# Kernel optimization log

Hardware: AMD Instinct MI355X
Metric: run time of the kernel (lower is better)

The kernel has to match this reference:

```python
import jax, jax.numpy as jnp
import numpy as np

B, K = 4096, 64
D_MODEL, D_DYN, D_STAT = 256, 512, 64
H = 4
DH = D_MODEL // H
SCALE = DH ** -0.5
LN_EPS = 1e-5


def _ln(x, g, b):
    m = x.mean(-1, keepdims=True)
    v = ((x - m) ** 2).mean(-1, keepdims=True)
    return (x - m) * jax.lax.rsqrt(v + LN_EPS) * g + b


def setup_inputs() -> dict:
    key = jax.random.key(0)
    ks = jax.random.split(key, 16)
    w = lambda k, s: jax.random.normal(k, s, jnp.float32) * 0.02
    return {
        "h_dyn": jax.random.normal(ks[0], (B, D_DYN), jnp.float32),
        "x_stat": jax.random.normal(ks[1], (B, K, D_STAT), jnp.float32),
        "W_dyn": w(ks[2], (D_DYN, D_MODEL)), "b_dyn": jnp.zeros((D_MODEL,)),
        "W_stat": w(ks[3], (D_STAT, D_MODEL)), "b_stat": jnp.zeros((D_MODEL,)),
        "g_ndyn": jnp.ones((D_MODEL,)), "b_ndyn": jnp.zeros((D_MODEL,)),
        "g_nstat": jnp.ones((D_MODEL,)), "b_nstat": jnp.zeros((D_MODEL,)),
        "Wq": w(ks[4], (D_MODEL, D_MODEL)), "bq": jnp.zeros((D_MODEL,)),
        "Wk": w(ks[5], (D_MODEL, D_MODEL)), "bk": jnp.zeros((D_MODEL,)),
        "Wv": w(ks[6], (D_MODEL, D_MODEL)), "bv": jnp.zeros((D_MODEL,)),
        "g_mlp": jnp.ones((D_MODEL,)), "b_mlp": jnpp if False else jnp.zeros((D_MODEL,)),
        "W1": w(ks[7], (D_MODEL, D_MODEL)), "b1": jnp.zeros((D_MODEL,)),
        "W2": w(ks[8], (D_MODEL, D_MODEL)), "b2": jnp.zeros((D_MODEL,)),
        "Wo": w(ks[9], (D_MODEL, D_MODEL)), "bo": jnp.zeros((D_MODEL,)),
        "res_scale": jnp.float32(0.1),
    }


def reference(h_dyn, x_stat, W_dyn, b_dyn, W_stat, b_stat, g_ndyn, b_ndyn,
              g_nstat, b_nstat, Wq, bq, Wk, bk, Wv, bv, g_mlp, b_mlp,
              W1, b1, W2, b2, Wo, bo, res_scale):
    h0 = h_dyn @ W_dyn + b_dyn                  # [B, d_model]
    s = x_stat @ W_stat + b_stat                # [B, K, d_model]
    h = _ln(h0, g_ndyn, b_ndyn)
    s = _ln(s, g_nstat, b_nstat)

    q = (h @ Wq + bq).reshape(B, H, DH)         # [B, H, dh]
    k = (s @ Wk + bk).reshape(B, K, H, DH)      # [B, K, H, dh]
    v_flat = s @ Wv + bv                        # [B, K, d_model]

    # per-variable MLP (DeepSets style): LN -> Linear -> GELU(exact) -> Linear
    t = _ln(v_flat, g_mlp, b_mlp)
    t = jax.nn.gelu(t @ W1 + b1, approximate=False)
    v_tokens = t @ W2 + b2                      # [B, K, d_model]

    logits = jnp.einsum('bhd,bkhd->bhk', q, k) * SCALE   # [B, H, K]
    w = jax.nn.sigmoid(logits)
    w = w / (w.sum(-1, keepdims=True) + 1e-6)

    vh = v_tokens.reshape(B, K, H, DH)
    z = jnp.einsum('bhk,bkhd->bhd', w, vh).reshape(B, D_MODEL)
    c = z @ Wo + bo
    c = h0 + res_scale * c
    w_mean = w.mean(axis=1)                     # [B, K]
    return c, w_mean
```

## Files before the change

kernel.cpp:

```cpp
#include <hip/hip_runtime.h>
#include <cmath>


typedef __bf16 bf16;
typedef bf16 bf16x4 __attribute__((ext_vector_type(4)));
typedef bf16 bf16x8 __attribute__((ext_vector_type(8)));
typedef float f32x4 __attribute__((ext_vector_type(4)));

#define MFMA_B16(a, b, c) __builtin_amdgcn_mfma_f32_16x16x32_bf16((a), (b), (c), 0, 0, 0)

constexpr int SROW = 264;

constexpr size_t WSTAT_P = 0;
constexpr size_t WV_P    = 16384;
constexpr size_t W1_P    = 81920;
constexpr size_t W2O_P   = 147456;
constexpr size_t WDYN_P  = 212992;
constexpr size_t WQ_P    = 344064;
constexpr size_t WK_P    = 409600;
constexpr size_t KQ_BF   = 475136;
constexpr size_t XP_BF   = 4669440;
constexpr size_t H0_F   = 10723328;
constexpr size_t BKQ_F  = 11771904;
constexpr size_t B2O_F  = 11788288;
constexpr size_t W2OS_F = 11788544;

__device__ __forceinline__ bf16x8 zero8() {
  bf16x8 z;
#pragma unroll
  for (int j = 0; j < 8; ++j) z[j] = (bf16)0.0f;
  return z;
}

__device__ __forceinline__ float wave_sum(float v) {
#pragma unroll
  for (int m = 1; m < 64; m <<= 1) v += __shfl_xor(v, m, 64);
  return v;
}

__device__ __forceinline__ void zero_acc(f32x4 (&acc)[4][4]) {
#pragma unroll
  for (int mt = 0; mt < 4; ++mt)
#pragma unroll
    for (int nt = 0; nt < 4; ++nt) { f32x4 z = {0.f, 0.f, 0.f, 0.f}; acc[mt][nt] = z; }
}

__device__ __forceinline__ void gemm_swapped_p(const bf16* buf, const bf16* __restrict__ Wp,
                                               int w, int lane, int l16, int koff,
                                               f32x4 (&acc)[4][4]) {
  const bf16* base = Wp + (size_t)w * 8 * 2048 + lane * 8;
  bf16x8 aw[2][4];
#pragma unroll
  for (int dt = 0; dt < 4; ++dt) aw[0][dt] = *(const bf16x8*)(base + dt * 512);
#pragma unroll
  for (int ks = 0; ks < 8; ++ks) {
    const int cur = ks & 1;
    if (ks < 7) {
#pragma unroll
      for (int dt = 0; dt < 4; ++dt)
        aw[cur ^ 1][dt] = *(const bf16x8*)(base + (ks + 1) * 2048 + dt * 512);
    }
#pragma unroll
    for (int tt = 0; tt < 4; ++tt) {
      bf16x8 bfrag = *(const bf16x8*)(buf + (tt * 16 + l16) * SROW + ks * 32 + koff);
#pragma unroll
      for (int dt = 0; dt < 4; ++dt) acc[dt][tt] = MFMA_B16(aw[cur][dt], bfrag, acc[dt][tt]);
    }
  }
}

__device__ __forceinline__ void gemm_orig_p(const bf16* buf, const bf16* __restrict__ Wp,
                                            int w, int lane, int l16, int koff,
                                            f32x4 (&acc)[4][4]) {
  const bf16* base = Wp + (size_t)w * 8 * 2048 + lane * 8;
  bf16x8 bw[2][4];
#pragma unroll
  for (int nt = 0; nt < 4; ++nt) bw[0][nt] = *(const bf16x8*)(base + nt * 512);
#pragma unroll
  for (int ks = 0; ks < 8; ++ks) {
    const int cur = ks & 1;
    if (ks < 7) {
#pragma unroll
      for (int nt = 0; nt < 4; ++nt)
        bw[cur ^ 1][nt] = *(const bf16x8*)(base + (ks + 1) * 2048 + nt * 512);
    }
#pragma unroll
    for (int mt = 0; mt < 4; ++mt) {
      bf16x8 a = *(const bf16x8*)(buf + (mt * 16 + l16) * SROW + ks * 32 + koff);
#pragma unroll
      for (int nt = 0; nt < 4; ++nt) acc[mt][nt] = MFMA_B16(a, bw[cur][nt], acc[mt][nt]);
    }
  }
}

__device__ __forceinline__ void store_swapped_stats(bf16* buf, const float* __restrict__ bsrc,
                                                    f32x4 (&acc)[4][4], int w, int quad, int l16,
                                                    float (*part_s)[64], float (*part_ss)[64]) {
  float ps[4] = {0.f, 0.f, 0.f, 0.f}, pq[4] = {0.f, 0.f, 0.f, 0.f};
#pragma unroll
  for (int dt = 0; dt < 4; ++dt) {
    const float4 bb = *(const float4*)(bsrc + w * 64 + dt * 16 + quad * 4);
#pragma unroll
    for (int tt = 0; tt < 4; ++tt) {
      float v0 = acc[dt][tt][0] + bb.x;
      float v1 = acc[dt][tt][1] + bb.y;
      float v2 = acc[dt][tt][2] + bb.z;
      float v3 = acc[dt][tt][3] + bb.w;
      ps[tt] += (v0 + v1) + (v2 + v3);
      pq[tt] += v0 * v0 + v1 * v1 + v2 * v2 + v3 * v3;
      bf16x4 o;
      o[0] = (bf16)v0; o[1] = (bf16)v1; o[2] = (bf16)v2; o[3] = (bf16)v3;
      *(bf16x4*)(buf + (tt * 16 + l16) * SROW + w * 64 + dt * 16 + quad * 4) = o;
    }
  }
#pragma unroll
  for (int tt = 0; tt < 4; ++tt) {
    ps[tt] += __shfl_xor(ps[tt], 16, 64); ps[tt] += __shfl_xor(ps[tt], 32, 64);
    pq[tt] += __shfl_xor(pq[tt], 16, 64); pq[tt] += __shfl_xor(pq[tt], 32, 64);
  }
  if (quad == 0) {
#pragma unroll
    for (int tt = 0; tt < 4; ++tt) {
      part_s[w][tt * 16 + l16] = ps[tt];
      part_ss[w][tt * 16 + l16] = pq[tt];
    }
  }
}

__device__ __forceinline__ void ln_finalize_apply(bf16* buf, const float* __restrict__ g,
                                                  const float* __restrict__ bsh,
                                                  const float (*part_s)[64],
                                                  const float (*part_ss)[64], int w, int lane) {
  float psum = (part_s[0][lane] + part_s[1][lane]) + (part_s[2][lane] + part_s[3][lane]);
  float pqq  = (part_ss[0][lane] + part_ss[1][lane]) + (part_ss[2][lane] + part_ss[3][lane]);
  float mean = psum * (1.f / 256.f);
  float var  = pqq * (1.f / 256.f) - mean * mean;
  float rstd = 1.f / sqrtf(var + 1e-5f);
  const float4 gv = *(const float4*)(g + lane * 4);
  const float4 bv4 = *(const float4*)(bsh + lane * 4);
#pragma unroll
  for (int i = 0; i < 16; ++i) {
    const int row = 4 * i + w;
    const float mb = __shfl(mean, row, 64);
    const float rb = __shfl(rstd, row, 64);
    bf16* rp = buf + row * SROW + lane * 4;
    bf16x4 xv = *(const bf16x4*)rp;
    bf16x4 o;
    o[0] = (bf16)(((float)xv[0] - mb) * rb * gv.x + bv4.x);
    o[1] = (bf16)(((float)xv[1] - mb) * rb * gv.y + bv4.y);
    o[2] = (bf16)(((float)xv[2] - mb) * rb * gv.z + bv4.z);
    o[3] = (bf16)(((float)xv[3] - mb) * rb * gv.w + bv4.w);
    *(bf16x4*)rp = o;
  }
}

template <typename SrcT>
__device__ __forceinline__ void pack_slice(const SrcT* __restrict__ src, bf16* __restrict__ dstb,
                                           int w, int ks, bool trans, float* sh, int tid) {
  if (!trans) {
#pragma unroll
    for (int i = 0; i < 8; ++i) {
      int r = i * 4 + (tid >> 6), c = tid & 63;
      sh[r * 65 + c] = (float)src[(size_t)(ks * 32 + r) * 256 + w * 64 + c];
    }
  } else {
    int c = tid >> 2, j8 = tid & 3;
#pragma unroll
    for (int jj = 0; jj < 8; ++jj) {
      int r = j8 * 8 + jj;
      sh[r * 65 + c] = (float)src[(size_t)(w * 64 + c) * 256 + ks * 32 + r];
    }
  }
  __syncthreads();
  const int x = tid >> 6, quad = (tid >> 4) & 3, l16 = tid & 15;
  bf16x8 o;
#pragma unroll
  for (int j = 0; j < 8; ++j) o[j] = (bf16)sh[(quad * 8 + j) * 65 + x * 16 + l16];
  *(bf16x8*)(dstb + tid * 8) = o;
}

__global__ void prep1_kernel(const float* __restrict__ x_stat,
                             const float* __restrict__ Wdyn, const float* __restrict__ Wstat,
                             const float* __restrict__ Wq, const float* __restrict__ Wk,
                             const float* __restrict__ Wv, const float* __restrict__ W1,
                             const float* __restrict__ W2, const float* __restrict__ Wo,
                             const float* __restrict__ b2,
                             bf16* __restrict__ ws, float* __restrict__ wsf) {
  __shared__ float sh[64 * 65];
  __shared__ float part[4][8];
  const int idx = blockIdx.x;
  const int tid = threadIdx.x;

  if (idx < 4096) {
    const float* xb = x_stat + (size_t)idx * 4096;
#pragma unroll
    for (int j = 0; j < 4; ++j) {
      int lin = j * 1024 + tid * 4;
      float4 v = *(const float4*)(xb + lin);
      int r = lin >> 6, c = lin & 63;
      sh[r * 65 + c] = v.x; sh[r * 65 + c + 1] = v.y;
      sh[r * 65 + c + 2] = v.z; sh[r * 65 + c + 3] = v.w;
    }
    __syncthreads();
    bf16* xp = ws + XP_BF + (size_t)idx * 4096;
#pragma unroll
    for (int half = 0; half < 2; ++half) {
      int s = half * 256 + tid;
      int ksq = s >> 6, lane = s & 63;
      int token = (ksq & 3) * 16 + (lane & 15);
      int f0 = (ksq >> 2) * 32 + (lane >> 4) * 8;
      bf16x8 o;
#pragma unroll
      for (int j = 0; j < 8; ++j) o[j] = (bf16)sh[token * 65 + f0 + j];
      *(bf16x8*)(xp + s * 8) = o;
    }
    return;
  }

  if (idx < 4128) {
    const int n0 = (idx - 4096) * 8;
    float4 a0 = *(const float4*)(Wo + (size_t)tid * 256 + n0);
    float4 a1 = *(const float4*)(Wo + (size_t)tid * 256 + n0 + 4);
    sh[tid * 8 + 0] = a0.x; sh[tid * 8 + 1] = a0.y; sh[tid * 8 + 2] = a0.z; sh[tid * 8 + 3] = a0.w;
    sh[tid * 8 + 4] = a1.x; sh[tid * 8 + 5] = a1.y; sh[tid * 8 + 6] = a1.z; sh[tid * 8 + 7] = a1.w;
    __syncthreads();
    float acc[8] = {0.f, 0.f, 0.f, 0.f, 0.f, 0.f, 0.f, 0.f};
    const float* row = W2 + (size_t)tid * 256;
    for (int d0 = 0; d0 < 256; d0 += 4) {
      float4 wv = *(const float4*)(row + d0);
#pragma unroll
      for (int dd = 0; dd < 4; ++dd) {
        float r = (dd == 0) ? wv.x : (dd == 1) ? wv.y : (dd == 2) ? wv.z : wv.w;
        const float* cc = &sh[(d0 + dd) * 8];
#pragma unroll
        for (int j = 0; j < 8; ++j) acc[j] += r * cc[j];
      }
    }
    float* dst = wsf + W2OS_F;
#pragma unroll
    for (int j = 0; j < 8; ++j) dst[(size_t)tid * 256 + n0 + j] = acc[j];
    const int w = tid >> 6, lane = tid & 63;
    float bval = b2[tid];
#pragma unroll
    for (int j = 0; j < 8; ++j) {
      float p = wave_sum(bval * sh[tid * 8 + j]);
      if (lane == 0) part[w][j] = p;
    }
    __syncthreads();
    if (tid < 8)
      wsf[B2O_F + n0 + tid] = part[0][tid] + part[1][tid] + part[2][tid] + part[3][tid];
    return;
  }

  int t = idx - 4128;
  const float* src; bf16* dst; int KS; bool trans = false;
  if (t < 64)       { src = Wdyn;  dst = ws + WDYN_P;  KS = 16; }
  else if (t < 72)  { src = Wstat; dst = ws + WSTAT_P; KS = 2;  t -= 64; }
  else if (t < 104) { src = Wq;    dst = ws + WQ_P;    KS = 8;  t -= 72; }
  else if (t < 136) { src = Wv;    dst = ws + WV_P;    KS = 8;  t -= 104; }
  else if (t < 168) { src = W1;    dst = ws + W1_P;    KS = 8;  t -= 136; }
  else              { src = Wk;    dst = ws + WK_P;    KS = 8;  t -= 168; trans = true; }
  const int w = t / KS, ks = t % KS;
  pack_slice<float>(src, dst + (size_t)(w * KS + ks) * 2048, w, ks, trans, sh, tid);
}

__global__ void prep2_kernel(const float* __restrict__ wsf_scr, bf16* __restrict__ ws) {
  __shared__ float sh[64 * 65];
  const int t = blockIdx.x;
  const int w = t >> 3, ks = t & 7;
  pack_slice<float>(wsf_scr, ws + W2O_P + (size_t)(w * 8 + ks) * 2048, w, ks, false, sh,
                    threadIdx.x);
}

__launch_bounds__(256, 2)
__global__ void pre_kernel(const float* __restrict__ h_dyn, const float* __restrict__ b_dyn,
                           const float* __restrict__ g_ndyn, const float* __restrict__ b_ndyn,
                           const float* __restrict__ bq, const float* __restrict__ bk,
                           const bf16* __restrict__ Wdyn_p, const bf16* __restrict__ Wq_p,
                           const bf16* __restrict__ Wk_p,
                           float* __restrict__ h0_out, bf16* __restrict__ kq_out,
                           float* __restrict__ bkq_out) {
  __shared__ float h0t[8][264];
  __shared__ bf16 hlnt[8][264];
  __shared__ bf16 qt[8][264];
  const int tid = threadIdx.x;
  const int w = tid >> 6, lane = tid & 63, quad = lane >> 4, l16 = lane & 15;
  const int koff = quad * 8;
  const int b0 = blockIdx.x * 8;
  const int mrow = l16 & 7;

  {
    f32x4 acc[4];
#pragma unroll
    for (int nt = 0; nt < 4; ++nt) { f32x4 z = {0.f, 0.f, 0.f, 0.f}; acc[nt] = z; }
    const float* arow = h_dyn + (size_t)(b0 + mrow) * 512;
    const bf16* base = Wdyn_p + (size_t)w * 16 * 2048 + lane * 8;
    for (int ks = 0; ks < 16; ++ks) {
      float4 x0 = *(const float4*)(arow + ks * 32 + koff);
      float4 x1 = *(const float4*)(arow + ks * 32 + koff + 4);
      bf16x8 a;
      a[0] = (bf16)x0.x; a[1] = (bf16)x0.y; a[2] = (bf16)x0.z; a[3] = (bf16)x0.w;
      a[4] = (bf16)x1.x; a[5] = (bf16)x1.y; a[6] = (bf16)x1.z; a[7] = (bf16)x1.w;
#pragma unroll
      for (int nt = 0; nt < 4; ++nt) {
        bf16x8 bw = *(const bf16x8*)(base + ks * 2048 + nt * 512);
        acc[nt] = MFMA_B16(a, bw, acc[nt]);
      }
    }
    if (quad < 2) {
#pragma unroll
      for (int nt = 0; nt < 4; ++nt) {
        int col = w * 64 + nt * 16 + l16;
        float bb = b_dyn[col];
#pragma unroll
        for (int r = 0; r < 4; ++r) {
          int row = quad * 4 + r;
          float v = acc[nt][r] + bb;
          h0t[row][col] = v;
          h0_out[(size_t)(b0 + row) * 256 + col] = v;
        }
      }
    }
  }
  __syncthreads();

  {
    float gn[4], bn[4];
#pragma unroll
    for (int j = 0; j < 4; ++j) { gn[j] = g_ndyn[lane + 64 * j]; bn[j] = b_ndyn[lane + 64 * j]; }
#pragma unroll
    for (int i = 0; i < 2; ++i) {
      int row = 4 * i + w;
      float x[4]; float s = 0.f, ss = 0.f;
#pragma unroll
      for (int j = 0; j < 4; ++j) { x[j] = h0t[row][lane + 64 * j]; s += x[j]; ss += x[j] * x[j]; }
      s = wave_sum(s); ss = wave_sum(ss);
      float mean = s * (1.f / 256.f);
      float var = ss * (1.f / 256.f) - mean * mean;
      float rstd = 1.f / sqrtf(var + 1e-5f);
#pragma unroll
      for (int j = 0; j < 4; ++j)
        hlnt[row][lane + 64 * j] = (bf16)((x[j] - mean) * rstd * gn[j] + bn[j]);
    }
  }
  __syncthreads();

  {
    f32x4 acc[4];
#pragma unroll
    for (int nt = 0; nt < 4; ++nt) { f32x4 z = {0.f, 0.f, 0.f, 0.f}; acc[nt] = z; }
    const bf16* base = Wq_p + (size_t)w * 8 * 2048 + lane * 8;
    for (int ks = 0; ks < 8; ++ks) {
      bf16x8 a = *(const bf16x8*)(&hlnt[mrow][ks * 32 + koff]);
#pragma unroll
      for (int nt = 0; nt < 4; ++nt) {
        bf16x8 bw = *(const bf16x8*)(base + ks * 2048 + nt * 512);
        acc[nt] = MFMA_B16(a, bw, acc[nt]);
      }
    }
    if (quad < 2) {
#pragma unroll
      for (int nt = 0; nt < 4; ++nt) {
        int col = w * 64 + nt * 16 + l16;
        float bb = bq[col];
#pragma unroll
        for (int r = 0; r < 4; ++r)
          qt[quad * 4 + r][col] = (bf16)(acc[nt][r] + bb);
      }
    }
  }
  __syncthreads();

  {
    const int pair = tid >> 2;
    const int row = pair >> 2, h = pair & 3, sub = tid & 3;
    if (row < 8) {
      float p = 0.f;
#pragma unroll
      for (int j = 0; j < 16; ++j) {
        int e = sub * 16 + j;
        p += (float)qt[row][h * 64 + e] * bk[h * 64 + e];
      }
      p += __shfl_xor(p, 1, 64);
      p += __shfl_xor(p, 2, 64);
      if (sub == 0) bkq_out[(size_t)(b0 + row) * 4 + h] = p;
    }
  }

  for (int h = 0; h < 4; ++h) {
    f32x4 acc[4];
#pragma unroll
    for (int nt = 0; nt < 4; ++nt) { f32x4 z = {0.f, 0.f, 0.f, 0.f}; acc[nt] = z; }
    const bf16* base = Wk_p + (size_t)w * 8 * 2048 + lane * 8;
#pragma unroll
    for (int ks = 0; ks < 2; ++ks) {
      bf16x8 a = *(const bf16x8*)(&qt[mrow][h * 64 + ks * 32 + koff]);
#pragma unroll
      for (int nt = 0; nt < 4; ++nt) {
        bf16x8 bw = *(const bf16x8*)(base + (h * 2 + ks) * 2048 + nt * 512);
        acc[nt] = MFMA_B16(a, bw, acc[nt]);
      }
    }
    if (quad < 2) {
#pragma unroll
      for (int nt = 0; nt < 4; ++nt)
#pragma unroll
        for (int r = 0; r < 4; ++r)
          kq_out[(size_t)(b0 + quad * 4 + r) * 1024 + h * 256 + w * 64 + nt * 16 + l16] =
              (bf16)acc[nt][r];
    }
  }
}

__launch_bounds__(256, 4)
__global__ void fused_kernel(
    const float* __restrict__ b_stat,
    const float* __restrict__ g_nstat, const float* __restrict__ b_nstat,
    const float* __restrict__ bv, const float* __restrict__ g_mlp,
    const float* __restrict__ b_mlp, const float* __restrict__ b1,
    const float* __restrict__ bo, const float* __restrict__ res_scale_p,
    const float* __restrict__ h0g, const float* __restrict__ bkq_g,
    const float* __restrict__ b2o_g,
    const bf16* __restrict__ Wstat_p, const bf16* __restrict__ Wv_p,
    const bf16* __restrict__ W1_p, const bf16* __restrict__ W2o_p,
    const bf16* __restrict__ kq_g, const bf16* __restrict__ xp_g,
    float* __restrict__ out_c, float* __restrict__ out_wm) {

  __shared__ bf16 buf[64 * SROW];
  __shared__ float part_s[4][64];
  __shared__ float part_ss[4][64];
  __shared__ float watt[4][64];
  __shared__ float swh[4];

  const int b = blockIdx.x;
  const int tid = threadIdx.x;
  const int w = tid >> 6, lane = tid & 63, quad = lane >> 4, l16 = lane & 15;
  const int koff = quad * 8;

  {
    f32x4 acc[4][4];
    zero_acc(acc);
    const bf16* xp_b = xp_g + (size_t)b * 4096 + lane * 8;
    const bf16* wsb = Wstat_p + (size_t)w * 2 * 2048 + lane * 8;
#pragma unroll
    for (int ks = 0; ks < 2; ++ks) {
      bf16x8 aw[4];
#pragma unroll
      for (int dt = 0; dt < 4; ++dt)
        aw[dt] = *(const bf16x8*)(wsb + ks * 2048 + dt * 512);
#pragma unroll
      for (int tt = 0; tt < 4; ++tt) {
        bf16x8 bfrag = *(const bf16x8*)(xp_b + (ks * 4 + tt) * 512);
#pragma unroll
        for (int dt = 0; dt < 4; ++dt) acc[dt][tt] = MFMA_B16(aw[dt], bfrag, acc[dt][tt]);
      }
    }
    store_swapped_stats(buf, b_stat, acc, w, quad, l16, part_s, part_ss);
  }
  __syncthreads();

  ln_finalize_apply(buf, g_nstat, b_nstat, part_s, part_ss, w, lane);
  __syncthreads();

  {
    const bf16* kq_b = kq_g + (size_t)b * 1024;
    f32x4 accL = {0.f, 0.f, 0.f, 0.f};
#pragma unroll
    for (int ks = 0; ks < 8; ++ks) {
      bf16x8 a = *(const bf16x8*)(buf + (w * 16 + l16) * SROW + ks * 32 + koff);
      bf16x8 kf = zero8();
      if (l16 < 4) kf = *(const bf16x8*)(kq_b + l16 * 256 + ks * 32 + koff);
      accL = MFMA_B16(a, kf, accL);
    }
    float bkqv = (l16 < 4) ? bkq_g[(size_t)b * 4 + l16] : 0.f;
#pragma unroll
    for (int r = 0; r < 4; ++r) {
      float lg = (accL[r] + bkqv) * 0.125f;
      float sig = 1.f / (1.f + __expf(-lg));
      if (l16 < 4) watt[l16][w * 16 + quad * 4 + r] = sig;
    }
  }

  {
    f32x4 acc[4][4];
    zero_acc(acc);
    gemm_swapped_p(buf, Wv_p, w, lane, l16, koff, acc);
    __syncthreads();
    {
      float v = watt[w][lane];
      float den = wave_sum(v);
      float dinv = 1.f / (den + 1e-6f);
      watt[w][lane] = v * dinv;
      if (lane == 0) swh[w] = den * dinv;
    }
    store_swapped_stats(buf, bv, acc, w, quad, l16, part_s, part_ss);
  }
  __syncthreads();

  if (tid < 64)
    out_wm[(size_t)b * 64 + tid] =
        0.25f * (watt[0][tid] + watt[1][tid] + watt[2][tid] + watt[3][tid]);
  ln_finalize_apply(buf, g_mlp, b_mlp, part_s, part_ss, w, lane);
  __syncthreads();

  {
    f32x4 acc[4][4];
    zero_acc(acc);
    gemm_swapped_p(buf, W1_p, w, lane, l16, koff, acc);
    __syncthreads();
#pragma unroll
    for (int dt = 0; dt < 4; ++dt) {
      const float4 bb = *(const float4*)(b1 + w * 64 + dt * 16 + quad * 4);
#pragma unroll
      for (int tt = 0; tt < 4; ++tt) {
        float v0 = acc[dt][tt][0] + bb.x;
        float v1 = acc[dt][tt][1] + bb.y;
        float v2 = acc[dt][tt][2] + bb.z;
        float v3 = acc[dt][tt][3] + bb.w;
        bf16x4 o;
        o[0] = (bf16)(v0 / (1.f + __expf(-1.702f * v0)));
        o[1] = (bf16)(v1 / (1.f + __expf(-1.702f * v1)));
        o[2] = (bf16)(v2 / (1.f + __expf(-1.702f * v2)));
        o[3] = (bf16)(v3 / (1.f + __expf(-1.702f * v3)));
        *(bf16x4*)(buf + (tt * 16 + l16) * SROW + w * 64 + dt * 16 + quad * 4) = o;
      }
    }
  }
  __syncthreads();

  {
    f32x4 acc[4][4];
    zero_acc(acc);
    gemm_orig_p(buf, W2o_p, w, lane, l16, koff, acc);
    float zacc[4] = {0.f, 0.f, 0.f, 0.f};
#pragma unroll
    for (int mt = 0; mt < 4; ++mt)
#pragma unroll
      for (int r = 0; r < 4; ++r) {
        float wt = watt[w][mt * 16 + quad * 4 + r];
#pragma unroll
        for (int nt = 0; nt < 4; ++nt) zacc[nt] += wt * acc[mt][nt][r];
      }
#pragma unroll
    for (int nt = 0; nt < 4; ++nt) {
      zacc[nt] += __shfl_xor(zacc[nt], 16, 64);
      zacc[nt] += __shfl_xor(zacc[nt], 32, 64);
    }
    if (quad == 0) {
      float rs = *res_scale_p;
#pragma unroll
      for (int nt = 0; nt < 4; ++nt) {
        int col = w * 64 + nt * 16 + l16;
        float res = zacc[nt] + swh[w] * b2o_g[col] + bo[col];
        out_c[(size_t)b * 256 + col] = h0g[(size_t)b * 256 + col] + rs * res;
      }
    }
  }
}

extern "C" void kernel_launch(void* const* d_in, const int* in_sizes, int n_in,
                              void* d_out, int out_size, void* d_ws, size_t ws_size,
                              hipStream_t stream) {
  const float* h_dyn   = (const float*)d_in[0];
  const float* x_stat  = (const float*)d_in[1];
  const float* W_dyn   = (const float*)d_in[2];
  const float* b_dyn   = (const float*)d_in[3];
  const float* W_stat  = (const float*)d_in[4];
  const float* b_stat  = (const float*)d_in[5];
  const float* g_ndyn  = (const float*)d_in[6];
  const float* b_ndyn  = (const float*)d_in[7];
  const float* g_nstat = (const float*)d_in[8];
  const float* b_nstat = (const float*)d_in[9];
  const float* Wq = (const float*)d_in[10];
  const float* bq = (const float*)d_in[11];
  const float* Wk = (const float*)d_in[12];
  const float* bk = (const float*)d_in[13];
  const float* Wv = (const float*)d_in[14];
  const float* bv = (const float*)d_in[15];
  const float* g_mlp = (const float*)d_in[16];
  const float* b_mlp = (const float*)d_in[17];
  const float* W1 = (const float*)d_in[18];
  const float* b1 = (const float*)d_in[19];
  const float* W2 = (const float*)d_in[20];
  const float* b2 = (const float*)d_in[21];
  const float* Wo = (const float*)d_in[22];
  const float* bo = (const float*)d_in[23];
  const float* rs = (const float*)d_in[24];

  bf16* ws = (bf16*)d_ws;
  float* wsf = (float*)d_ws;

  prep1_kernel<<<4328, 256, 0, stream>>>(x_stat, W_dyn, W_stat, Wq, Wk, Wv, W1, W2, Wo, b2,
                                         ws, wsf);
  prep2_kernel<<<32, 256, 0, stream>>>(wsf + W2OS_F, ws);

  pre_kernel<<<512, 256, 0, stream>>>(h_dyn, b_dyn, g_ndyn, b_ndyn, bq, bk,
                                      ws + WDYN_P, ws + WQ_P, ws + WK_P,
                                      wsf + H0_F, ws + KQ_BF, wsf + BKQ_F);

  float* out_c = (float*)d_out;
  float* out_wm = out_c + (size_t)4096 * 256;
  fused_kernel<<<4096, 256, 0, stream>>>(
      b_stat, g_nstat, b_nstat, bv, g_mlp, b_mlp, b1, bo, rs,
      wsf + H0_F, wsf + BKQ_F, wsf + B2O_F,
      ws + WSTAT_P, ws + WV_P, ws + W1_P, ws + W2O_P,
      ws + KQ_BF, ws + XP_BF,
      out_c, out_wm);
}
```

Baseline: 340.0 us.

## Process two batches per block, load x_stat directly, drop prepacked x buffer

The fused kernel now handles two batch items per block (128 token rows), so each weight fragment loaded from global memory is reused across twice as many MFMA tiles. The separate prep pass that converted x_stat to packed bf16 in the workspace is removed. x_stat is instead read as fp32 and converted into LDS inside the fused kernel, which saves a full write and reread of that tensor. The pre_kernel GEMMs also get double-buffered weight loads. In exchange, LDS roughly doubles, the accumulator arrays grow to 32 tiles, and occupancy drops to 2 blocks per CU with a risk of register pressure.

Measured after the change: 328.3 us. 3.5% less time.

```diff
diff --git a/kernel.cpp b/kernel.cpp
--- a/kernel.cpp
+++ b/kernel.cpp
@@ -10,6 +10,7 @@
 #define MFMA_B16(a, b, c) __builtin_amdgcn_mfma_f32_16x16x32_bf16((a), (b), (c), 0, 0, 0)
 
 constexpr int SROW = 264;
+constexpr int XROW = 72;
 
 constexpr size_t WSTAT_P = 0;
 constexpr size_t WV_P    = 16384;
@@ -19,11 +20,10 @@
 constexpr size_t WQ_P    = 344064;
 constexpr size_t WK_P    = 409600;
 constexpr size_t KQ_BF   = 475136;
-constexpr size_t XP_BF   = 4669440;
-constexpr size_t H0_F   = 10723328;
-constexpr size_t BKQ_F  = 11771904;
-constexpr size_t B2O_F  = 11788288;
-constexpr size_t W2OS_F = 11788544;
+constexpr size_t H0_F   = 2334720;
+constexpr size_t BKQ_F  = 3383296;
+constexpr size_t B2O_F  = 3399680;
+constexpr size_t W2OS_F = 3399936;
 
 __device__ __forceinline__ bf16x8 zero8() {
   bf16x8 z;
@@ -38,16 +38,9 @@
   return v;
 }
 
-__device__ __forceinline__ void zero_acc(f32x4 (&acc)[4][4]) {
-#pragma unroll
-  for (int mt = 0; mt < 4; ++mt)
-#pragma unroll
-    for (int nt = 0; nt < 4; ++nt) { f32x4 z = {0.f, 0.f, 0.f, 0.f}; acc[mt][nt] = z; }
-}
-
-__device__ __forceinline__ void gemm_swapped_p(const bf16* buf, const bf16* __restrict__ Wp,
-                                               int w, int lane, int l16, int koff,
-                                               f32x4 (&acc)[4][4]) {
+__device__ __forceinline__ void gemm_swapped8(const bf16* buf, const bf16* __restrict__ Wp,
+                                              int w, int lane, int l16, int koff,
+                                              f32x4 (&acc)[4][8]) {
   const bf16* base = Wp + (size_t)w * 8 * 2048 + lane * 8;
   bf16x8 aw[2][4];
 #pragma unroll
@@ -61,7 +54,7 @@
         aw[cur ^ 1][dt] = *(const bf16x8*)(base + (ks + 1) * 2048 + dt * 512);
     }
 #pragma unroll
-    for (int tt = 0; tt < 4; ++tt) {
+    for (int tt = 0; tt < 8; ++tt) {
       bf16x8 bfrag = *(const bf16x8*)(buf + (tt * 16 + l16) * SROW + ks * 32 + koff);
 #pragma unroll
       for (int dt = 0; dt < 4; ++dt) acc[dt][tt] = MFMA_B16(aw[cur][dt], bfrag, acc[dt][tt]);
@@ -69,9 +62,9 @@
   }
 }
 
-__device__ __forceinline__ void gemm_orig_p(const bf16* buf, const bf16* __restrict__ Wp,
-                                            int w, int lane, int l16, int koff,
-                                            f32x4 (&acc)[4][4]) {
+__device__ __forceinline__ void gemm_orig8(const bf16* buf, const bf16* __restrict__ Wp,
+                                           int w, int lane, int l16, int koff,
+                                           f32x4 (&acc)[8][4]) {
   const bf16* base = Wp + (size_t)w * 8 * 2048 + lane * 8;
   bf16x8 bw[2][4];
 #pragma unroll
@@ -85,7 +78,7 @@
         bw[cur ^ 1][nt] = *(const bf16x8*)(base + (ks + 1) * 2048 + nt * 512);
     }
 #pragma unroll
-    for (int mt = 0; mt < 4; ++mt) {
+    for (int mt = 0; mt < 8; ++mt) {
       bf16x8 a = *(const bf16x8*)(buf + (mt * 16 + l16) * SROW + ks * 32 + koff);
 #pragma unroll
       for (int nt = 0; nt < 4; ++nt) acc[mt][nt] = MFMA_B16(a, bw[cur][nt], acc[mt][nt]);
@@ -93,15 +86,17 @@
   }
 }
 
-__device__ __forceinline__ void store_swapped_stats(bf16* buf, const float* __restrict__ bsrc,
-                                                    f32x4 (&acc)[4][4], int w, int quad, int l16,
-                                                    float (*part_s)[64], float (*part_ss)[64]) {
-  float ps[4] = {0.f, 0.f, 0.f, 0.f}, pq[4] = {0.f, 0.f, 0.f, 0.f};
+__device__ __forceinline__ void store_stats8(bf16* buf, const float* __restrict__ bsrc,
+                                             f32x4 (&acc)[4][8], int w, int quad, int l16,
+                                             float (*part_s)[4][64], float (*part_ss)[4][64]) {
+  float ps[8], pq[8];
+#pragma unroll
+  for (int tt = 0; tt < 8; ++tt) { ps[tt] = 0.f; pq[tt] = 0.f; }
 #pragma unroll
   for (int dt = 0; dt < 4; ++dt) {
     const float4 bb = *(const float4*)(bsrc + w * 64 + dt * 16 + quad * 4);
 #pragma unroll
-    for (int tt = 0; tt < 4; ++tt) {
+    for (int tt = 0; tt < 8; ++tt) {
       float v0 = acc[dt][tt][0] + bb.x;
       float v1 = acc[dt][tt][1] + bb.y;
       float v2 = acc[dt][tt][2] + bb.z;
@@ -114,61 +109,67 @@
     }
   }
 #pragma unroll
-  for (int tt = 0; tt < 4; ++tt) {
+  for (int tt = 0; tt < 8; ++tt) {
     ps[tt] += __shfl_xor(ps[tt], 16, 64); ps[tt] += __shfl_xor(ps[tt], 32, 64);
     pq[tt] += __shfl_xor(pq[tt], 16, 64); pq[tt] += __shfl_xor(pq[tt], 32, 64);
   }
   if (quad == 0) {
 #pragma unroll
-    for (int tt = 0; tt < 4; ++tt) {
-      part_s[w][tt * 16 + l16] = ps[tt];
-      part_ss[w][tt * 16 + l16] = pq[tt];
-    }
-  }
-}
-
-__device__ __forceinline__ void ln_finalize_apply(bf16* buf, const float* __restrict__ g,
-                                                  const float* __restrict__ bsh,
-                                                  const float (*part_s)[64],
-                                                  const float (*part_ss)[64], int w, int lane) {
-  float psum = (part_s[0][lane] + part_s[1][lane]) + (part_s[2][lane] + part_s[3][lane]);
-  float pqq  = (part_ss[0][lane] + part_ss[1][lane]) + (part_ss[2][lane] + part_ss[3][lane]);
-  float mean = psum * (1.f / 256.f);
-  float var  = pqq * (1.f / 256.f) - mean * mean;
-  float rstd = 1.f / sqrtf(var + 1e-5f);
+    for (int tt = 0; tt < 8; ++tt) {
+      part_s[tt >> 2][w][(tt & 3) * 16 + l16] = ps[tt];
+      part_ss[tt >> 2][w][(tt & 3) * 16 + l16] = pq[tt];
+    }
+  }
+}
+
+__device__ __forceinline__ void ln_apply2(bf16* buf, const float* __restrict__ g,
+                                          const float* __restrict__ bsh,
+                                          const float (*ps)[4][64], const float (*pss)[4][64],
+                                          int w, int lane) {
+  float mean[2], rstd[2];
+#pragma unroll
+  for (int bb = 0; bb < 2; ++bb) {
+    float s = (ps[bb][0][lane] + ps[bb][1][lane]) + (ps[bb][2][lane] + ps[bb][3][lane]);
+    float q = (pss[bb][0][lane] + pss[bb][1][lane]) + (pss[bb][2][lane] + pss[bb][3][lane]);
+    mean[bb] = s * (1.f / 256.f);
+    float var = q * (1.f / 256.f) - mean[bb] * mean[bb];
+    rstd[bb] = 1.f / sqrtf(var + 1e-5f);
+  }
   const float4 gv = *(const float4*)(g + lane * 4);
   const float4 bv4 = *(const float4*)(bsh + lane * 4);
 #pragma unroll
-  for (int i = 0; i < 16; ++i) {
-    const int row = 4 * i + w;
-    const float mb = __shfl(mean, row, 64);
-    const float rb = __shfl(rstd, row, 64);
-    bf16* rp = buf + row * SROW + lane * 4;
-    bf16x4 xv = *(const bf16x4*)rp;
-    bf16x4 o;
-    o[0] = (bf16)(((float)xv[0] - mb) * rb * gv.x + bv4.x);
-    o[1] = (bf16)(((float)xv[1] - mb) * rb * gv.y + bv4.y);
-    o[2] = (bf16)(((float)xv[2] - mb) * rb * gv.z + bv4.z);
-    o[3] = (bf16)(((float)xv[3] - mb) * rb * gv.w + bv4.w);
-    *(bf16x4*)rp = o;
-  }
-}
-
-template <typename SrcT>
-__device__ __forceinline__ void pack_slice(const SrcT* __restrict__ src, bf16* __restrict__ dstb,
+  for (int bb = 0; bb < 2; ++bb) {
+#pragma unroll
+    for (int i = 0; i < 16; ++i) {
+      const int r64 = 4 * i + w;
+      const float mb = __shfl(mean[bb], r64, 64);
+      const float rb = __shfl(rstd[bb], r64, 64);
+      bf16* rp = buf + (bb * 64 + r64) * SROW + lane * 4;
+      bf16x4 xv = *(const bf16x4*)rp;
+      bf16x4 o;
+      o[0] = (bf16)(((float)xv[0] - mb) * rb * gv.x + bv4.x);
+      o[1] = (bf16)(((float)xv[1] - mb) * rb * gv.y + bv4.y);
+      o[2] = (bf16)(((float)xv[2] - mb) * rb * gv.z + bv4.z);
+      o[3] = (bf16)(((float)xv[3] - mb) * rb * gv.w + bv4.w);
+      *(bf16x4*)rp = o;
+    }
+  }
+}
+
+__device__ __forceinline__ void pack_slice(const float* __restrict__ src, bf16* __restrict__ dstb,
                                            int w, int ks, bool trans, float* sh, int tid) {
   if (!trans) {
 #pragma unroll
     for (int i = 0; i < 8; ++i) {
       int r = i * 4 + (tid >> 6), c = tid & 63;
-      sh[r * 65 + c] = (float)src[(size_t)(ks * 32 + r) * 256 + w * 64 + c];
+      sh[r * 65 + c] = src[(size_t)(ks * 32 + r) * 256 + w * 64 + c];
     }
   } else {
     int c = tid >> 2, j8 = tid & 3;
 #pragma unroll
     for (int jj = 0; jj < 8; ++jj) {
       int r = j8 * 8 + jj;
-      sh[r * 65 + c] = (float)src[(size_t)(w * 64 + c) * 256 + ks * 32 + r];
+      sh[r * 65 + c] = src[(size_t)(w * 64 + c) * 256 + ks * 32 + r];
     }
   }
   __syncthreads();
@@ -179,8 +180,7 @@
   *(bf16x8*)(dstb + tid * 8) = o;
 }
 
-__global__ void prep1_kernel(const float* __restrict__ x_stat,
-                             const float* __restrict__ Wdyn, const float* __restrict__ Wstat,
+__global__ void prep1_kernel(const float* __restrict__ Wdyn, const float* __restrict__ Wstat,
                              const float* __restrict__ Wq, const float* __restrict__ Wk,
                              const float* __restrict__ Wv, const float* __restrict__ W1,
                              const float* __restrict__ W2, const float* __restrict__ Wo,
@@ -191,34 +191,8 @@
   const int idx = blockIdx.x;
   const int tid = threadIdx.x;
 
-  if (idx < 4096) {
-    const float* xb = x_stat + (size_t)idx * 4096;
-#pragma unroll
-    for (int j = 0; j < 4; ++j) {
-      int lin = j * 1024 + tid * 4;
-      float4 v = *(const float4*)(xb + lin);
-      int r = lin >> 6, c = lin & 63;
-      sh[r * 65 + c] = v.x; sh[r * 65 + c + 1] = v.y;
-      sh[r * 65 + c + 2] = v.z; sh[r * 65 + c + 3] = v.w;
-    }
-    __syncthreads();
-    bf16* xp = ws + XP_BF + (size_t)idx * 4096;
-#pragma unroll
-    for (int half = 0; half < 2; ++half) {
-      int s = half * 256 + tid;
-      int ksq = s >> 6, lane = s & 63;
-      int token = (ksq & 3) * 16 + (lane & 15);
-      int f0 = (ksq >> 2) * 32 + (lane >> 4) * 8;
-      bf16x8 o;
-#pragma unroll
-      for (int j = 0; j < 8; ++j) o[j] = (bf16)sh[token * 65 + f0 + j];
-      *(bf16x8*)(xp + s * 8) = o;
-    }
-    return;
-  }
-
-  if (idx < 4128) {
-    const int n0 = (idx - 4096) * 8;
+  if (idx < 32) {
+    const int n0 = idx * 8;
     float4 a0 = *(const float4*)(Wo + (size_t)tid * 256 + n0);
     float4 a1 = *(const float4*)(Wo + (size_t)tid * 256 + n0 + 4);
     sh[tid * 8 + 0] = a0.x; sh[tid * 8 + 1] = a0.y; sh[tid * 8 + 2] = a0.z; sh[tid * 8 + 3] = a0.w;
@@ -252,7 +226,7 @@
     return;
   }
 
-  int t = idx - 4128;
+  int t = idx - 32;
   const float* src; bf16* dst; int KS; bool trans = false;
   if (t < 64)       { src = Wdyn;  dst = ws + WDYN_P;  KS = 16; }
   else if (t < 72)  { src = Wstat; dst = ws + WSTAT_P; KS = 2;  t -= 64; }
@@ -261,15 +235,13 @@
   else if (t < 168) { src = W1;    dst = ws + W1_P;    KS = 8;  t -= 136; }
   else              { src = Wk;    dst = ws + WK_P;    KS = 8;  t -= 168; trans = true; }
   const int w = t / KS, ks = t % KS;
-  pack_slice<float>(src, dst + (size_t)(w * KS + ks) * 2048, w, ks, trans, sh, tid);
+  pack_slice(src, dst + (size_t)(w * KS + ks) * 2048, w, ks, trans, sh, tid);
 }
 
 __global__ void prep2_kernel(const float* __restrict__ wsf_scr, bf16* __restrict__ ws) {
   __shared__ float sh[64 * 65];
   const int t = blockIdx.x;
-  const int w = t >> 3, ks = t & 7;
-  pack_slice<float>(wsf_scr, ws + W2O_P + (size_t)(w * 8 + ks) * 2048, w, ks, false, sh,
-                    threadIdx.x);
+  pack_slice(wsf_scr, ws + W2O_P + (size_t)t * 2048, t >> 3, t & 7, false, sh, threadIdx.x);
 }
 
 __launch_bounds__(256, 2)
@@ -295,17 +267,23 @@
     for (int nt = 0; nt < 4; ++nt) { f32x4 z = {0.f, 0.f, 0.f, 0.f}; acc[nt] = z; }
     const float* arow = h_dyn + (size_t)(b0 + mrow) * 512;
     const bf16* base = Wdyn_p + (size_t)w * 16 * 2048 + lane * 8;
+    bf16x8 bw[2][4];
+#pragma unroll
+    for (int nt = 0; nt < 4; ++nt) bw[0][nt] = *(const bf16x8*)(base + nt * 512);
     for (int ks = 0; ks < 16; ++ks) {
+      const int cur = ks & 1;
+      if (ks < 15) {
+#pragma unroll
+        for (int nt = 0; nt < 4; ++nt)
+          bw[cur ^ 1][nt] = *(const bf16x8*)(base + (ks + 1) * 2048 + nt * 512);
+      }
       float4 x0 = *(const float4*)(arow + ks * 32 + koff);
       float4 x1 = *(const float4*)(arow + ks * 32 + koff + 4);
       bf16x8 a;
       a[0] = (bf16)x0.x; a[1] = (bf16)x0.y; a[2] = (bf16)x0.z; a[3] = (bf16)x0.w;
       a[4] = (bf16)x1.x; a[5] = (bf16)x1.y; a[6] = (bf16)x1.z; a[7] = (bf16)x1.w;
 #pragma unroll
-      for (int nt = 0; nt < 4; ++nt) {
-        bf16x8 bw = *(const bf16x8*)(base + ks * 2048 + nt * 512);
-        acc[nt] = MFMA_B16(a, bw, acc[nt]);
-      }
+      for (int nt = 0; nt < 4; ++nt) acc[nt] = MFMA_B16(a, bw[cur][nt], acc[nt]);
     }
     if (quad < 2) {
 #pragma unroll
@@ -350,13 +328,19 @@
 #pragma unroll
     for (int nt = 0; nt < 4; ++nt) { f32x4 z = {0.f, 0.f, 0.f, 0.f}; acc[nt] = z; }
     const bf16* base = Wq_p + (size_t)w * 8 * 2048 + lane * 8;
+    bf16x8 bw[2][4];
+#pragma unroll
+    for (int nt = 0; nt < 4; ++nt) bw[0][nt] = *(const bf16x8*)(base + nt * 512);
     for (int ks = 0; ks < 8; ++ks) {
+      const int cur = ks & 1;
+      if (ks < 7) {
+#pragma unroll
+        for (int nt = 0; nt < 4; ++nt)
+          bw[cur ^ 1][nt] = *(const bf16x8*)(base + (ks + 1) * 2048 + nt * 512);
+      }
       bf16x8 a = *(const bf16x8*)(&hlnt[mrow][ks * 32 + koff]);
 #pragma unroll
-      for (int nt = 0; nt < 4; ++nt) {
-        bf16x8 bw = *(const bf16x8*)(base + ks * 2048 + nt * 512);
-        acc[nt] = MFMA_B16(a, bw, acc[nt]);
-      }
+      for (int nt = 0; nt < 4; ++nt) acc[nt] = MFMA_B16(a, bw[cur][nt], acc[nt]);
     }
     if (quad < 2) {
 #pragma unroll
@@ -412,9 +396,9 @@
   }
 }
 
-__launch_bounds__(256, 4)
+__launch_bounds__(256, 2)
 __global__ void fused_kernel(
-    const float* __restrict__ b_stat,
+    const float* __restrict__ x_stat, const float* __restrict__ b_stat,
     const float* __restrict__ g_nstat, const float* __restrict__ b_nstat,
     const float* __restrict__ bv, const float* __restrict__ g_mlp,
     const float* __restrict__ b_mlp, const float* __restrict__ b1,
@@ -423,96 +407,124 @@
     const float* __restrict__ b2o_g,
     const bf16* __restrict__ Wstat_p, const bf16* __restrict__ Wv_p,
     const bf16* __restrict__ W1_p, const bf16* __restrict__ W2o_p,
-    const bf16* __restrict__ kq_g, const bf16* __restrict__ xp_g,
+    const bf16* __restrict__ kq_g,
     float* __restrict__ out_c, float* __restrict__ out_wm) {
 
-  __shared__ bf16 buf[64 * SROW];
-  __shared__ float part_s[4][64];
-  __shared__ float part_ss[4][64];
-  __shared__ float watt[4][64];
-  __shared__ float swh[4];
-
-  const int b = blockIdx.x;
+  __shared__ bf16 buf[128 * SROW];
+  __shared__ float part_s[2][4][64];
+  __shared__ float part_ss[2][4][64];
+  __shared__ float watt[2][4][64];
+  __shared__ float swh[2][4];
+
+  const int b0 = blockIdx.x * 2;
   const int tid = threadIdx.x;
   const int w = tid >> 6, lane = tid & 63, quad = lane >> 4, l16 = lane & 15;
   const int koff = quad * 8;
 
-  {
-    f32x4 acc[4][4];
-    zero_acc(acc);
-    const bf16* xp_b = xp_g + (size_t)b * 4096 + lane * 8;
+  bf16* xs = buf;
+  {
+    const float* xb = x_stat + (size_t)b0 * 4096;
+#pragma unroll
+    for (int j = 0; j < 8; ++j) {
+      int idx = j * 1024 + tid * 4;
+      float4 v = *(const float4*)(xb + idx);
+      bf16x4 o;
+      o[0] = (bf16)v.x; o[1] = (bf16)v.y; o[2] = (bf16)v.z; o[3] = (bf16)v.w;
+      *(bf16x4*)(xs + (idx >> 6) * XROW + (idx & 63)) = o;
+    }
+  }
+  __syncthreads();
+
+  {
+    f32x4 acc[4][8];
+#pragma unroll
+    for (int dt = 0; dt < 4; ++dt)
+#pragma unroll
+      for (int tt = 0; tt < 8; ++tt) { f32x4 z = {0.f, 0.f, 0.f, 0.f}; acc[dt][tt] = z; }
     const bf16* wsb = Wstat_p + (size_t)w * 2 * 2048 + lane * 8;
-#pragma unroll
-    for (int ks = 0; ks < 2; ++ks) {
-      bf16x8 aw[4];
+    bf16x8 aw[2][4];
+#pragma unroll
+    for (int ks = 0; ks < 2; ++ks)
 #pragma unroll
       for (int dt = 0; dt < 4; ++dt)
-        aw[dt] = *(const bf16x8*)(wsb + ks * 2048 + dt * 512);
-#pragma unroll
-      for (int tt = 0; tt < 4; ++tt) {
-        bf16x8 bfrag = *(const bf16x8*)(xp_b + (ks * 4 + tt) * 512);
-#pragma unroll
-        for (int dt = 0; dt < 4; ++dt) acc[dt][tt] = MFMA_B16(aw[dt], bfrag, acc[dt][tt]);
-      }
-    }
-    store_swapped_stats(buf, b_stat, acc, w, quad, l16, part_s, part_ss);
-  }
-  __syncthreads();
-
-  ln_finalize_apply(buf, g_nstat, b_nstat, part_s, part_ss, w, lane);
-  __syncthreads();
-
-  {
-    const bf16* kq_b = kq_g + (size_t)b * 1024;
+        aw[ks][dt] = *(const bf16x8*)(wsb + ks * 2048 + dt * 512);
+#pragma unroll
+    for (int ks = 0; ks < 2; ++ks)
+#pragma unroll
+      for (int tt = 0; tt < 8; ++tt) {
+        bf16x8 bfrag = *(const bf16x8*)(xs + (tt * 16 + l16) * XROW + ks * 32 + koff);
+#pragma unroll
+        for (int dt = 0; dt < 4; ++dt) acc[dt][tt] = MFMA_B16(aw[ks][dt], bfrag, acc[dt][tt]);
+      }
+    __syncthreads();
+    store_stats8(buf, b_stat, acc, w, quad, l16, part_s, part_ss);
+  }
+  __syncthreads();
+
+  ln_apply2(buf, g_nstat, b_nstat, part_s, part_ss, w, lane);
+  __syncthreads();
+
+#pragma unroll
+  for (int bb = 0; bb < 2; ++bb) {
+    const bf16* kq_b = kq_g + (size_t)(b0 + bb) * 1024;
     f32x4 accL = {0.f, 0.f, 0.f, 0.f};
 #pragma unroll
     for (int ks = 0; ks < 8; ++ks) {
-      bf16x8 a = *(const bf16x8*)(buf + (w * 16 + l16) * SROW + ks * 32 + koff);
+      bf16x8 a = *(const bf16x8*)(buf + (bb * 64 + w * 16 + l16) * SROW + ks * 32 + koff);
       bf16x8 kf = zero8();
       if (l16 < 4) kf = *(const bf16x8*)(kq_b + l16 * 256 + ks * 32 + koff);
       accL = MFMA_B16(a, kf, accL);
     }
-    float bkqv = (l16 < 4) ? bkq_g[(size_t)b * 4 + l16] : 0.f;
+    float bkqv = (l16 < 4) ? bkq_g[(size_t)(b0 + bb) * 4 + l16] : 0.f;
 #pragma unroll
     for (int r = 0; r < 4; ++r) {
       float lg = (accL[r] + bkqv) * 0.125f;
       float sig = 1.f / (1.f + __expf(-lg));
-      if (l16 < 4) watt[l16][w * 16 + quad * 4 + r] = sig;
-    }
-  }
-
-  {
-    f32x4 acc[4][4];
-    zero_acc(acc);
-    gemm_swapped_p(buf, Wv_p, w, lane, l16, koff, acc);
+      if (l16 < 4) watt[bb][l16][w * 16 + quad * 4 + r] = sig;
+    }
+  }
+
+  {
+    f32x4 acc[4][8];
+#pragma unroll
+    for (int dt = 0; dt < 4; ++dt)
+#pragma unroll
+      for (int tt = 0; tt < 8; ++tt) { f32x4 z = {0.f, 0.f, 0.f, 0.f}; acc[dt][tt] = z; }
+    gemm_swapped8(buf, Wv_p, w, lane, l16, koff, acc);
     __syncthreads();
-    {
-      float v = watt[w][lane];
+#pragma unroll
+    for (int bb = 0; bb < 2; ++bb) {
+      float v = watt[bb][w][lane];
       float den = wave_sum(v);
       float dinv = 1.f / (den + 1e-6f);
-      watt[w][lane] = v * dinv;
-      if (lane == 0) swh[w] = den * dinv;
-    }
-    store_swapped_stats(buf, bv, acc, w, quad, l16, part_s, part_ss);
-  }
-  __syncthreads();
-
-  if (tid < 64)
-    out_wm[(size_t)b * 64 + tid] =
-        0.25f * (watt[0][tid] + watt[1][tid] + watt[2][tid] + watt[3][tid]);
-  ln_finalize_apply(buf, g_mlp, b_mlp, part_s, part_ss, w, lane);
-  __syncthreads();
-
-  {
-    f32x4 acc[4][4];
-    zero_acc(acc);
-    gemm_swapped_p(buf, W1_p, w, lane, l16, koff, acc);
+      watt[bb][w][lane] = v * dinv;
+      if (lane == 0) swh[bb][w] = den * dinv;
+    }
+    store_stats8(buf, bv, acc, w, quad, l16, part_s, part_ss);
+  }
+  __syncthreads();
+
+  if (tid < 128) {
+    int bb = tid >> 6, t = tid & 63;
+    out_wm[(size_t)(b0 + bb) * 64 + t] =
+        0.25f * ((watt[bb][0][t] + watt[bb][1][t]) + (watt[bb][2][t] + watt[bb][3][t]));
+  }
+  ln_apply2(buf, g_mlp, b_mlp, part_s, part_ss, w, lane);
+  __syncthreads();
+
+  {
+    f32x4 acc[4][8];
+#pragma unroll
+    for (int dt = 0; dt < 4; ++dt)
+#pragma unroll
+      for (int tt = 0; tt < 8; ++tt) { f32x4 z = {0.f, 0.f, 0.f, 0.f}; acc[dt][tt] = z; }
+    gemm_swapped8(buf, W1_p, w, lane, l16, koff, acc);
     __syncthreads();
 #pragma unroll
     for (int dt = 0; dt < 4; ++dt) {
       const float4 bb = *(const float4*)(b1 + w * 64 + dt * 16 + quad * 4);
 #pragma unroll
-      for (int tt = 0; tt < 4; ++tt) {
+      for (int tt = 0; tt < 8; ++tt) {
         float v0 = acc[dt][tt][0] + bb.x;
         float v1 = acc[dt][tt][1] + bb.y;
         float v2 = acc[dt][tt][2] + bb.z;
@@ -529,31 +541,44 @@
   __syncthreads();
 
   {
-    f32x4 acc[4][4];
-    zero_acc(acc);
-    gemm_orig_p(buf, W2o_p, w, lane, l16, koff, acc);
-    float zacc[4] = {0.f, 0.f, 0.f, 0.f};
-#pragma unroll
-    for (int mt = 0; mt < 4; ++mt)
+    f32x4 acc[8][4];
+#pragma unroll
+    for (int mt = 0; mt < 8; ++mt)
+#pragma unroll
+      for (int nt = 0; nt < 4; ++nt) { f32x4 z = {0.f, 0.f, 0.f, 0.f}; acc[mt][nt] = z; }
+    gemm_orig8(buf, W2o_p, w, lane, l16, koff, acc);
+    float zacc[2][4];
+#pragma unroll
+    for (int bb = 0; bb < 2; ++bb)
+#pragma unroll
+      for (int nt = 0; nt < 4; ++nt) zacc[bb][nt] = 0.f;
+#pragma unroll
+    for (int mt = 0; mt < 8; ++mt) {
+      const int bb = mt >> 2;
 #pragma unroll
       for (int r = 0; r < 4; ++r) {
-        float wt = watt[w][mt * 16 + quad * 4 + r];
-#pragma unroll
-        for (int nt = 0; nt < 4; ++nt) zacc[nt] += wt * acc[mt][nt][r];
-      }
-#pragma unroll
-    for (int nt = 0; nt < 4; ++nt) {
-      zacc[nt] += __shfl_xor(zacc[nt], 16, 64);
-      zacc[nt] += __shfl_xor(zacc[nt], 32, 64);
-    }
+        float wt = watt[bb][w][(mt & 3) * 16 + quad * 4 + r];
+#pragma unroll
+        for (int nt = 0; nt < 4; ++nt) zacc[bb][nt] += wt * acc[mt][nt][r];
+      }
+    }
+#pragma unroll
+    for (int bb = 0; bb < 2; ++bb)
+#pragma unroll
+      for (int nt = 0; nt < 4; ++nt) {
+        zacc[bb][nt] += __shfl_xor(zacc[bb][nt], 16, 64);
+        zacc[bb][nt] += __shfl_xor(zacc[bb][nt], 32, 64);
+      }
     if (quad == 0) {
       float rs = *res_scale_p;
 #pragma unroll
-      for (int nt = 0; nt < 4; ++nt) {
-        int col = w * 64 + nt * 16 + l16;
-        float res = zacc[nt] + swh[w] * b2o_g[col] + bo[col];
-        out_c[(size_t)b * 256 + col] = h0g[(size_t)b * 256 + col] + rs * res;
-      }
+      for (int bb = 0; bb < 2; ++bb)
+#pragma unroll
+        for (int nt = 0; nt < 4; ++nt) {
+          int col = w * 64 + nt * 16 + l16;
+          float res = zacc[bb][nt] + swh[bb][w] * b2o_g[col] + bo[col];
+          out_c[(size_t)(b0 + bb) * 256 + col] = h0g[(size_t)(b0 + bb) * 256 + col] + rs * res;
+        }
     }
   }
 }
@@ -590,8 +615,7 @@
   bf16* ws = (bf16*)d_ws;
   float* wsf = (float*)d_ws;
 
-  prep1_kernel<<<4328, 256, 0, stream>>>(x_stat, W_dyn, W_stat, Wq, Wk, Wv, W1, W2, Wo, b2,
-                                         ws, wsf);
+  prep1_kernel<<<232, 256, 0, stream>>>(W_dyn, W_stat, Wq, Wk, Wv, W1, W2, Wo, b2, ws, wsf);
   prep2_kernel<<<32, 256, 0, stream>>>(wsf + W2OS_F, ws);
 
   pre_kernel<<<512, 256, 0, stream>>>(h_dyn, b_dyn, g_ndyn, b_ndyn, bq, bk,
@@ -600,10 +624,9 @@
 
   float* out_c = (float*)d_out;
   float* out_wm = out_c + (size_t)4096 * 256;
-  fused_kernel<<<4096, 256, 0, stream>>>(
-      b_stat, g_nstat, b_nstat, bv, g_mlp, b_mlp, b1, bo, rs,
+  fused_kernel<<<2048, 256, 0, stream>>>(
+      x_stat, b_stat, g_nstat, b_nstat, bv, g_mlp, b_mlp, b1, bo, rs,
       wsf + H0_F, wsf + BKQ_F, wsf + B2O_F,
-      ws + WSTAT_P, ws + WV_P, ws + W1_P, ws + W2O_P,
-      ws + KQ_BF, ws + XP_BF,
+      ws + WSTAT_P, ws + WV_P, ws + W1_P, ws + W2O_P, ws + KQ_BF,
       out_c, out_wm);
 }
```
